# Performance work log

Hardware: AMD Instinct MI355X
Metric: run time of the kernel (lower is better)

Reference implementation:

```python
import jax, jax.numpy as jnp
import numpy as np

B, N_PER, D = 128, 512, 128        # graphs, nodes per graph, feature width
N = B * N_PER                      # 65536 total nodes
E = 524288                         # total edges (avg degree 8)
KS = (410, 328, 263)               # ceil(0.8*512), ceil(0.8*410), ceil(0.8*328)


def setup_inputs() -> dict:
    key = jax.random.key(0)
    ks = jax.random.split(key, 20)
    p = lambda k, shape: jax.random.normal(k, shape, jnp.float32) * 0.05
    rng = np.random.default_rng(0)
    g = rng.integers(0, B, size=E)
    s = rng.integers(0, N_PER, size=E)
    t = rng.integers(0, N_PER, size=E)
    edge_index = jnp.asarray(np.stack([g * N_PER + s, g * N_PER + t]).astype(np.int32))
    inp = {
        'x': jax.random.normal(ks[0], (N, 1, D), jnp.float32),
        'edge_index': edge_index,
    }
    i = 1
    for l in (1, 2, 3):
        inp[f'conv{l}_wl'] = p(ks[i], (D, D)); i += 1   # SAGEConv lin_l (neighbors) weight
        inp[f'conv{l}_bl'] = p(ks[i], (D,));  i += 1   # SAGEConv lin_l bias
        inp[f'conv{l}_wr'] = p(ks[i], (D, D)); i += 1   # SAGEConv lin_r (root) weight
        inp[f'pool{l}_w'] = p(ks[i], (D,));   i += 1   # TopKPooling score vector
    inp['lin1_w'] = p(ks[13], (128, 256)); inp['lin1_b'] = p(ks[14], (128,))
    inp['lin2_w'] = p(ks[15], (64, 128));  inp['lin2_b'] = p(ks[16], (64,))
    inp['lin3_w'] = p(ks[17], (1, 64));    inp['lin3_b'] = p(ks[18], (1,))
    return inp


def _sage(x, node_mask, src, dst, wl, bl, wr):
    # SAGEConv, mean aggregation: lin_l(mean_{j->i} x_j) + lin_r(x_i)
    em = (node_mask[src] & node_mask[dst]).astype(x.dtype)   # [E] valid-edge mask
    msum = jax.ops.segment_sum(x[src] * em[:, None], dst, num_segments=N)
    deg = jax.ops.segment_sum(em, dst, num_segments=N)
    mean = msum / jnp.maximum(deg, 1.0)[:, None]
    return mean @ wl.T + bl + x @ wr.T


def _topk_pool(x, node_mask, w, k):
    # TopKPooling: score = x.w/||w||; keep top-k per graph; gate kept x by tanh(score)
    score = (x @ w) / (jnp.linalg.norm(w) + 1e-16)           # [N]
    score = jnp.where(node_mask, score, -jnp.inf)
    _, idx = jax.lax.top_k(score.reshape(B, N_PER), k)       # [B, k] within-graph ids
    nm = jnp.zeros((B, N_PER), bool).at[jnp.arange(B)[:, None], idx].set(True).reshape(-1)
    x = jnp.where(nm[:, None], x * jnp.tanh(score)[:, None], 0.0)
    return x, nm


def _readout(x, node_mask, k):
    # cat([global_max_pool, global_mean_pool]) over the k surviving nodes per graph
    xb = x.reshape(B, N_PER, -1)
    mb = node_mask.reshape(B, N_PER, 1)
    gmax = jnp.max(jnp.where(mb, xb, -jnp.inf), axis=1)
    gmean = jnp.sum(jnp.where(mb, xb, 0.0), axis=1) / k
    return jnp.concatenate([gmax, gmean], axis=1)            # [B, 2D]


def _forward(edge_index, x, conv1_wl, conv1_bl, conv1_wr, pool1_w,
             conv2_wl, conv2_bl, conv2_wr, pool2_w,
             conv3_wl, conv3_bl, conv3_wr, pool3_w,
             lin1_w, lin1_b, lin2_w, lin2_b, lin3_w, lin3_b):
    src, dst = edge_index[0], edge_index[1]
    h = x[:, 0, :]                                           # x.squeeze(1) -> [N, D]
    nm = jnp.ones((N,), bool)
    layers = ((conv1_wl, conv1_bl, conv1_wr, pool1_w),
              (conv2_wl, conv2_bl, conv2_wr, pool2_w),
              (conv3_wl, conv3_bl, conv3_wr, pool3_w))
    reads = []
    for (wl, bl, wr, pw), k in zip(layers, KS):
        h = jax.nn.relu(_sage(h, nm, src, dst, wl, bl, wr))
        h, nm = _topk_pool(h, nm, pw, k)
        reads.append(_readout(h, nm, float(k)))
    z = reads[0] + reads[1] + reads[2]                       # [B, 256]
    z = jax.nn.relu(z @ lin1_w.T + lin1_b)
    z = jax.nn.relu(z @ lin2_w.T + lin2_b)
    # dropout p=0.5 is a no-op at eval time
    return jax.nn.sigmoid(z @ lin3_w.T + lin3_b)[:, 0]       # [B]


def reference(x, edge_index, conv1_wl, conv1_bl, conv1_wr, pool1_w,
              conv2_wl, conv2_bl, conv2_wr, pool2_w,
              conv3_wl, conv3_bl, conv3_wr, pool3_w,
              lin1_w, lin1_b, lin2_w, lin2_b, lin3_w, lin3_b):
    return _forward(edge_index, x, conv1_wl, conv1_bl, conv1_wr, pool1_w,
                    conv2_wl, conv2_bl, conv2_wr, pool2_w,
                    conv3_wl, conv3_bl, conv3_wr, pool3_w,
                    lin1_w, lin1_b, lin2_w, lin2_b, lin3_w, lin3_b)
```

## Files before the change

kernel.cpp:

```cpp
#include <hip/hip_runtime.h>
#include <math.h>

#define NND 65536
#define NPER 512
#define NGR 128
#define DD 128
#define NED 524288

typedef __attribute__((ext_vector_type(8))) short short8;
typedef __attribute__((ext_vector_type(4))) float f32x4;

__device__ __forceinline__ unsigned short f2b(float f) {
  unsigned u = __float_as_uint(f);
  return (unsigned short)((u + 0x7FFFu + ((u >> 16) & 1u)) >> 16);
}
__device__ __forceinline__ float b2f(unsigned short h) {
  return __uint_as_float(((unsigned)h) << 16);
}


__global__ __launch_bounds__(256) void init_kernel(int* __restrict__ counts,
                                                   float2* __restrict__ tm) {
  int i = blockIdx.x * 256 + threadIdx.x;
  counts[i] = 0;
  tm[i] = make_float2(1.f, 1.f);
}

__global__ __launch_bounds__(256) void hist_kernel(const int* __restrict__ ei,
                                                   int* __restrict__ counts) {
  int e = blockIdx.x * 256 + threadIdx.x;
  atomicAdd(&counts[ei[NED + e]], 1);
}

__global__ __launch_bounds__(1024) void scan_kernel(const int* __restrict__ counts,
                                                    int* __restrict__ off,
                                                    int* __restrict__ cursor) {
  __shared__ int part[1024];
  int t = threadIdx.x;
  int base = t * 64;
  int s = 0;
  const int4* c4 = (const int4*)(counts + base);
  for (int i = 0; i < 16; ++i) {
    int4 v = c4[i];
    s += v.x + v.y + v.z + v.w;
  }
  part[t] = s;
  __syncthreads();
  for (int d = 1; d < 1024; d <<= 1) {
    int v = (t >= d) ? part[t - d] : 0;
    __syncthreads();
    part[t] += v;
    __syncthreads();
  }
  int run = (t == 0) ? 0 : part[t - 1];
  for (int i = 0; i < 64; ++i) {
    off[base + i] = run;
    cursor[base + i] = run;
    run += counts[base + i];
  }
  if (t == 1023) off[NND] = run;
}

__global__ __launch_bounds__(256) void scatter_kernel(const int* __restrict__ ei,
                                                      int* __restrict__ cursor,
                                                      int* __restrict__ ssrc) {
  int e = blockIdx.x * 256 + threadIdx.x;
  int dst = ei[NED + e];
  int pos = atomicAdd(&cursor[dst], 1);
  ssrc[pos] = ei[e];
}


__global__ __launch_bounds__(256) void prepw_kernel(
    const float* __restrict__ wl0, const float* __restrict__ wr0,
    const float* __restrict__ wl1, const float* __restrict__ wr1,
    const float* __restrict__ wl2, const float* __restrict__ wr2,
    unsigned short* __restrict__ Whi, unsigned short* __restrict__ Wlo) {
  const float* wls[3] = {wl0, wl1, wl2};
  const float* wrs[3] = {wr0, wr1, wr2};
  int e = blockIdx.x * 256 + threadIdx.x;
  int l = e >> 15;
  int o = e & 32767;
  int j = o & 7;
  int lane = (o >> 3) & 63;
  int nt = (o >> 9) & 7;
  int kc = o >> 12;
  int li = lane & 15, q = lane >> 4;
  int n = nt * 16 + li;
  int k = kc * 32 + q * 8 + j;
  const float* src = (k < 128) ? wls[l] : wrs[l];
  float v = src[n * DD + (k & 127)];
  unsigned short hi = f2b(v);
  float lo = v - b2f(hi);
  Whi[e] = hi;
  Wlo[e] = f2b(lo);
}


template <int CM>
__global__ __launch_bounds__(256) void agg_kernel_t(const float* __restrict__ x,
                                                    const float2* __restrict__ tm,
                                                    const int* __restrict__ off,
                                                    const int* __restrict__ ssrc,
                                                    float* __restrict__ mean) {
  const int wave = threadIdx.x >> 6;
  const int lane = threadIdx.x & 63;
  const int half = lane >> 5;
  const int l = lane & 31;
  const int bid = blockIdx.x;
  const int xcd = bid & 7;
  const int slot = bid >> 3;
  const int graph = xcd * 16 + (slot >> 7);
  const int within = slot & 127;
  const int dst = graph * NPER + within * 4 + wave;

  if (CM && tm[dst].x == 0.f) {
    if (lane < 32) *(float4*)(mean + (size_t)dst * DD + l * 4) = make_float4(0.f, 0.f, 0.f, 0.f);
    return;
  }
  const int beg = off[dst], end = off[dst + 1];
  float4 acc = make_float4(0.f, 0.f, 0.f, 0.f);
  int deg = 0;
  for (int base = beg; base < end; base += 64) {
    const int n = min(64, end - base);
    int sv = 0;
    float tv = 0.f;
    int live = 0;
    if (lane < n) {
      sv = ssrc[base + lane];
      if (CM) {
        const float2 mt = tm[sv];
        live = (mt.x != 0.f);
        tv = mt.y;
      }
    }
    if (CM)
      deg += (int)__popcll(__ballot(live));
    else
      deg += n;
    int j = half;
    for (; j + 6 < n; j += 8) {
      const int s0 = __shfl(sv, j);
      const int s1 = __shfl(sv, j + 2);
      const int s2 = __shfl(sv, j + 4);
      const int s3 = __shfl(sv, j + 6);
      const float4 v0 = *(const float4*)(x + (size_t)s0 * DD + l * 4);
      const float4 v1 = *(const float4*)(x + (size_t)s1 * DD + l * 4);
      const float4 v2 = *(const float4*)(x + (size_t)s2 * DD + l * 4);
      const float4 v3 = *(const float4*)(x + (size_t)s3 * DD + l * 4);
      if (CM) {
        const float t0 = __shfl(tv, j), t1 = __shfl(tv, j + 2);
        const float t2 = __shfl(tv, j + 4), t3 = __shfl(tv, j + 6);
        acc.x += v0.x * t0 + v1.x * t1 + v2.x * t2 + v3.x * t3;
        acc.y += v0.y * t0 + v1.y * t1 + v2.y * t2 + v3.y * t3;
        acc.z += v0.z * t0 + v1.z * t1 + v2.z * t2 + v3.z * t3;
        acc.w += v0.w * t0 + v1.w * t1 + v2.w * t2 + v3.w * t3;
      } else {
        acc.x += v0.x + v1.x + v2.x + v3.x;
        acc.y += v0.y + v1.y + v2.y + v3.y;
        acc.z += v0.z + v1.z + v2.z + v3.z;
        acc.w += v0.w + v1.w + v2.w + v3.w;
      }
    }
    for (; j < n; j += 2) {
      const int s = __shfl(sv, j);
      const float4 v = *(const float4*)(x + (size_t)s * DD + l * 4);
      if (CM) {
        const float t = __shfl(tv, j);
        acc.x += v.x * t;
        acc.y += v.y * t;
        acc.z += v.z * t;
        acc.w += v.w * t;
      } else {
        acc.x += v.x;
        acc.y += v.y;
        acc.z += v.z;
        acc.w += v.w;
      }
    }
  }
  acc.x += __shfl(acc.x, lane ^ 32);
  acc.y += __shfl(acc.y, lane ^ 32);
  acc.z += __shfl(acc.z, lane ^ 32);
  acc.w += __shfl(acc.w, lane ^ 32);
  const float inv = 1.f / (float)max(deg, 1);
  if (lane < 32) {
    float4 m;
    m.x = acc.x * inv;
    m.y = acc.y * inv;
    m.z = acc.z * inv;
    m.w = acc.w * inv;
    *(float4*)(mean + (size_t)dst * DD + l * 4) = m;
  }
}


#define GBM 64

template <int SCALE>
__global__ __launch_bounds__(256) void gemm_kernel_t(
    const float* __restrict__ Amean, const float* __restrict__ Ax,
    const float2* __restrict__ tmp,
    const unsigned short* __restrict__ Whi, const unsigned short* __restrict__ Wlo,
    const float* __restrict__ bias, const float* __restrict__ pw,
    float* __restrict__ outp, float* __restrict__ sraw) {
  __shared__ short Ah[2048];
  __shared__ short Al[2048];
  __shared__ float s_sp[4][GBM];
  const int tid = threadIdx.x;
  const int wv = tid >> 6;
  const int lane = tid & 63;
  const int q = lane >> 4;
  const int li = lane & 15;
  const int row0 = blockIdx.x * GBM;

  int sdst[2];
#pragma unroll
  for (int i = 0; i < 2; ++i) {
    const int id = tid + i * 256;
    const int r = id >> 3;
    const int kb = (id & 7) << 2;
    sdst[i] = ((r >> 4) * 64 + (kb >> 3) * 16 + (r & 15)) * 8 + (kb & 7);
  }

  f32x4 acc[4][2];
#pragma unroll
  for (int m = 0; m < 4; ++m)
#pragma unroll
    for (int n = 0; n < 2; ++n) acc[m][n] = (f32x4){0.f, 0.f, 0.f, 0.f};

  float4 pa[2];
  short8 pbh[2], pbl[2];

#define LOADA(KC)                                                                    \
  {                                                                                  \
    const float* Asrc = ((KC) < 4) ? Amean : Ax;                                     \
    const int cb = ((KC) & 3) * 32;                                                  \
    _Pragma("unroll") for (int i = 0; i < 2; ++i) {                                  \
      const int id = tid + i * 256;                                                  \
      pa[i] = *(const float4*)(Asrc + (size_t)(row0 + (id >> 3)) * DD + cb + ((id & 7) << 2)); \
      if (SCALE && (KC) >= 4) {                                                      \
        const float tt = tmp[row0 + (id >> 3)].y;                                    \
        pa[i].x *= tt; pa[i].y *= tt; pa[i].z *= tt; pa[i].w *= tt;                   \
      }                                                                              \
    }                                                                                \
  }
#define LOADB(KC)                                                                    \
  {                                                                                  \
    _Pragma("unroll") for (int n = 0; n < 2; ++n) {                                  \
      const int ga = (((KC)*8 + wv * 2 + n) * 64 + lane) * 8;                        \
      pbh[n] = *(const short8*)(Whi + ga);                                           \
      pbl[n] = *(const short8*)(Wlo + ga);                                           \
    }                                                                                \
  }

  LOADA(0) LOADB(0)

#pragma unroll
  for (int kc = 0; kc < 8; ++kc) {
#pragma unroll
    for (int i = 0; i < 2; ++i) {
      ushort4 hv, lv;
      hv.x = f2b(pa[i].x); lv.x = f2b(pa[i].x - b2f(hv.x));
      hv.y = f2b(pa[i].y); lv.y = f2b(pa[i].y - b2f(hv.y));
      hv.z = f2b(pa[i].z); lv.z = f2b(pa[i].z - b2f(hv.z));
      hv.w = f2b(pa[i].w); lv.w = f2b(pa[i].w - b2f(hv.w));
      *(ushort4*)(Ah + sdst[i]) = hv;
      *(ushort4*)(Al + sdst[i]) = lv;
    }
    short8 bh[2], bl[2];
    bh[0] = pbh[0]; bh[1] = pbh[1];
    bl[0] = pbl[0]; bl[1] = pbl[1];
    __syncthreads();
    short8 ah[4], al[4];
#pragma unroll
    for (int m = 0; m < 4; ++m) {
      ah[m] = *(const short8*)(Ah + (m * 64 + lane) * 8);
      al[m] = *(const short8*)(Al + (m * 64 + lane) * 8);
    }
    if (kc < 7) { LOADA(kc + 1) LOADB(kc + 1) }
#pragma unroll
    for (int m = 0; m < 4; ++m)
#pragma unroll
      for (int n = 0; n < 2; ++n) {
        acc[m][n] = __builtin_amdgcn_mfma_f32_16x16x32_bf16(ah[m], bh[n], acc[m][n], 0, 0, 0);
        acc[m][n] = __builtin_amdgcn_mfma_f32_16x16x32_bf16(ah[m], bl[n], acc[m][n], 0, 0, 0);
        acc[m][n] = __builtin_amdgcn_mfma_f32_16x16x32_bf16(al[m], bh[n], acc[m][n], 0, 0, 0);
      }
    __syncthreads();
  }
#undef LOADA
#undef LOADB

  const int c0 = wv * 32 + li;
  const int c1 = wv * 32 + 16 + li;
  const float b0 = bias[c0], b1 = bias[c1];
  const float p0 = pw[c0], p1 = pw[c1];
  float sp[16];
#pragma unroll
  for (int m = 0; m < 4; ++m) {
#pragma unroll
    for (int i = 0; i < 4; ++i) {
      const int r = row0 + m * 16 + q * 4 + i;
      const float v0 = fmaxf(acc[m][0][i] + b0, 0.f);
      const float v1 = fmaxf(acc[m][1][i] + b1, 0.f);
      outp[(size_t)r * DD + c0] = v0;
      outp[(size_t)r * DD + c1] = v1;
      sp[m * 4 + i] = v0 * p0 + v1 * p1;
    }
  }
#pragma unroll
  for (int e = 0; e < 16; ++e) {
    sp[e] += __shfl_xor(sp[e], 1);
    sp[e] += __shfl_xor(sp[e], 2);
    sp[e] += __shfl_xor(sp[e], 4);
    sp[e] += __shfl_xor(sp[e], 8);
  }
  if (li == 0) {
#pragma unroll
    for (int e = 0; e < 16; ++e) s_sp[wv][(e >> 2) * 16 + q * 4 + (e & 3)] = sp[e];
  }
  __syncthreads();
  if (tid < GBM)
    sraw[row0 + tid] = s_sp[0][tid] + s_sp[1][tid] + s_sp[2][tid] + s_sp[3][tid];
}


__global__ __launch_bounds__(256) void pool_kernel(const float* __restrict__ h,
                                                   const float* __restrict__ sraw,
                                                   const float* __restrict__ pw,
                                                   const float2* __restrict__ tmP,
                                                   float2* __restrict__ tmN,
                                                   float* __restrict__ zp,
                                                   const int kk) {
  __shared__ float s_sc[NPER];
  __shared__ float s_t[128];
  __shared__ unsigned char s_sel[128];
  __shared__ int s_rk[256];
  __shared__ float4 red4[512];
  __shared__ float s_norm;
  const int b = blockIdx.x;
  const int g = b >> 2;
  const int q = b & 3;
  const int tid = threadIdx.x;
  const int lane = tid & 63;

  if (tid < 64) {
    const float v0 = pw[lane], v1 = pw[lane + 64];
    float p = v0 * v0 + v1 * v1;
#pragma unroll
    for (int o = 32; o > 0; o >>= 1) p += __shfl_down(p, o);
    if (lane == 0) s_norm = 1.f / (sqrtf(p) + 1e-16f);
  }
  __syncthreads();
  const float inv_norm = s_norm;
#pragma unroll
  for (int i = 0; i < 2; ++i) {
    const int n = tid + i * 256;
    const int node = g * NPER + n;
    s_sc[n] = (tmP[node].x != 0.f) ? sraw[node] * inv_norm : -INFINITY;
  }
  __syncthreads();

  {
    const int n = q * 128 + (tid & 127);
    const int jb = (tid >> 7) * 256;
    const float s = s_sc[n];
    int rank = 0;
    for (int j = jb; j < jb + 256; ++j) {
      const float sj = s_sc[j];
      rank += (sj > s || (sj == s && j < n)) ? 1 : 0;
    }
    s_rk[tid] = rank;
  }
  __syncthreads();
  if (tid < 128) {
    const int n = q * 128 + tid;
    const int rank = s_rk[tid] + s_rk[tid + 128];
    const int sel = (rank < kk) ? 1 : 0;
    const float s = s_sc[n];
    const float t = sel ? tanhf(s) : 0.f;
    tmN[g * NPER + n] = make_float2(sel ? 1.f : 0.f, t);
    s_sel[tid] = (unsigned char)sel;
    s_t[tid] = t;
  }
  __syncthreads();

  const int c = tid & 31;
  const int r = tid >> 5;
  float4 pmax = make_float4(-INFINITY, -INFINITY, -INFINITY, -INFINITY);
  float4 psum = make_float4(0.f, 0.f, 0.f, 0.f);
  const size_t nbase = (size_t)g * NPER + q * 128;
  const float4* h4 = (const float4*)h;
  for (int i = 0; i < 16; ++i) {
    const int nl = r + 8 * i;
    if (s_sel[nl]) {
      float4 v = h4[(nbase + nl) * 32 + c];
      const float t = s_t[nl];
      v.x *= t; v.y *= t; v.z *= t; v.w *= t;
      pmax.x = fmaxf(pmax.x, v.x);
      pmax.y = fmaxf(pmax.y, v.y);
      pmax.z = fmaxf(pmax.z, v.z);
      pmax.w = fmaxf(pmax.w, v.w);
      psum.x += v.x; psum.y += v.y; psum.z += v.z; psum.w += v.w;
    }
  }
  red4[r * 32 + c] = pmax;
  red4[256 + r * 32 + c] = psum;
  __syncthreads();
  if (tid < 32) {
    float4 m = red4[tid];
    float4 sm = red4[256 + tid];
#pragma unroll
    for (int rr = 1; rr < 8; ++rr) {
      const float4 a = red4[rr * 32 + tid];
      const float4 s2 = red4[256 + rr * 32 + tid];
      m.x = fmaxf(m.x, a.x); m.y = fmaxf(m.y, a.y);
      m.z = fmaxf(m.z, a.z); m.w = fmaxf(m.w, a.w);
      sm.x += s2.x; sm.y += s2.y; sm.z += s2.z; sm.w += s2.w;
    }
    *(float4*)(zp + (size_t)b * 256 + tid * 4) = m;
    *(float4*)(zp + (size_t)b * 256 + 128 + tid * 4) = sm;
  }
}


__global__ __launch_bounds__(128) void mlp_kernel(const float* __restrict__ zpart,
                                                  const float* __restrict__ w1,
                                                  const float* __restrict__ b1,
                                                  const float* __restrict__ w2,
                                                  const float* __restrict__ b2,
                                                  const float* __restrict__ w3,
                                                  const float* __restrict__ b3,
                                                  float* __restrict__ out,
                                                  const float ik0, const float ik1,
                                                  const float ik2) {
  __shared__ float z[256];
  __shared__ float h1[128];
  __shared__ float h2[64];
  const int g = blockIdx.x;
  const int t = threadIdx.x;
  const float iks[3] = {ik0, ik1, ik2};
  float zmax = 0.f, zmean = 0.f;
#pragma unroll
  for (int l = 0; l < 3; ++l) {
    const float* zp = zpart + ((size_t)l * 512 + g * 4) * 256;
    zmax += fmaxf(fmaxf(zp[t], zp[256 + t]), fmaxf(zp[512 + t], zp[768 + t]));
    zmean += (zp[128 + t] + zp[384 + t] + zp[640 + t] + zp[896 + t]) * iks[l];
  }
  z[t] = zmax;
  z[128 + t] = zmean;
  __syncthreads();
  float a = b1[t];
  for (int k = 0; k < 256; ++k) a = fmaf(z[k], w1[t * 256 + k], a);
  h1[t] = fmaxf(a, 0.f);
  __syncthreads();
  if (t < 64) {
    float a2 = b2[t];
    for (int k = 0; k < 128; ++k) a2 = fmaf(h1[k], w2[t * 128 + k], a2);
    h2[t] = fmaxf(a2, 0.f);
  }
  __syncthreads();
  if (t == 0) {
    float a3 = b3[0];
    for (int k = 0; k < 64; ++k) a3 = fmaf(h2[k], w3[k], a3);
    out[g] = 1.f / (1.f + expf(-a3));
  }
}


extern "C" void kernel_launch(void* const* d_in, const int* in_sizes, int n_in,
                              void* d_out, int out_size, void* d_ws, size_t ws_size,
                              hipStream_t stream) {
  (void)in_sizes; (void)n_in; (void)out_size; (void)ws_size;
  const float* x_in = (const float*)d_in[0];
  const int* ei = (const int*)d_in[1];
  const float* wl[3] = {(const float*)d_in[2], (const float*)d_in[6], (const float*)d_in[10]};
  const float* cbl[3] = {(const float*)d_in[3], (const float*)d_in[7], (const float*)d_in[11]};
  const float* wr[3] = {(const float*)d_in[4], (const float*)d_in[8], (const float*)d_in[12]};
  const float* pw[3] = {(const float*)d_in[5], (const float*)d_in[9], (const float*)d_in[13]};
  const float* l1w = (const float*)d_in[14];
  const float* l1b = (const float*)d_in[15];
  const float* l2w = (const float*)d_in[16];
  const float* l2b = (const float*)d_in[17];
  const float* l3w = (const float*)d_in[18];
  const float* l3b = (const float*)d_in[19];
  float* out = (float*)d_out;

  char* w = (char*)d_ws;
  int* counts = (int*)(w + 0 * (1 << 20));
  int* off = (int*)(w + 1 * (1 << 20));
  int* cursor = (int*)(w + 2 * (1 << 20));
  float* sraw = (float*)(w + 2 * (1 << 20));
  float2* tmA = (float2*)(w + 3 * (1 << 20));
  float2* tmB = (float2*)(w + 3 * (1 << 20) + (1 << 19));
  float* zpart = (float*)(w + 4 * (1 << 20));
  unsigned short* Whi = (unsigned short*)(w + 5 * (1 << 20) + (1 << 19));
  unsigned short* Wlo = (unsigned short*)(w + 5 * (1 << 20) + 3 * (1 << 18));
  int* ssrc = (int*)(w + 6 * (1 << 20));
  float* mean = (float*)(w + (size_t)8 * (1 << 20));
  float* hA = (float*)(w + (size_t)40 * (1 << 20));
  float* hB = (float*)(w + (size_t)72 * (1 << 20));

  init_kernel<<<NND / 256, 256, 0, stream>>>(counts, tmA);
  hist_kernel<<<NED / 256, 256, 0, stream>>>(ei, counts);
  scan_kernel<<<1, 1024, 0, stream>>>(counts, off, cursor);
  scatter_kernel<<<NED / 256, 256, 0, stream>>>(ei, cursor, ssrc);
  prepw_kernel<<<384, 256, 0, stream>>>(wl[0], wr[0], wl[1], wr[1], wl[2], wr[2], Whi, Wlo);

  const int ks[3] = {410, 328, 263};
  const float* xl = x_in;
  float* houts[3] = {hA, hB, hA};
  float2* tprev[3] = {tmA, tmB, tmA};
  float2* tnext[3] = {tmB, tmA, tmB};
  for (int l = 0; l < 3; ++l) {
    float* hout = houts[l];
    if (l == 0) {
      agg_kernel_t<0><<<NND / 4, 256, 0, stream>>>(xl, tprev[l], off, ssrc, mean);
      gemm_kernel_t<0><<<NND / GBM, 256, 0, stream>>>(mean, xl, tprev[l],
                                                      Whi + (size_t)l * 32768,
                                                      Wlo + (size_t)l * 32768, cbl[l], pw[l],
                                                      hout, sraw);
    } else {
      agg_kernel_t<1><<<NND / 4, 256, 0, stream>>>(xl, tprev[l], off, ssrc, mean);
      gemm_kernel_t<1><<<NND / GBM, 256, 0, stream>>>(mean, xl, tprev[l],
                                                      Whi + (size_t)l * 32768,
                                                      Wlo + (size_t)l * 32768, cbl[l], pw[l],
                                                      hout, sraw);
    }
    pool_kernel<<<NGR * 4, 256, 0, stream>>>(hout, sraw, pw[l], tprev[l], tnext[l],
                                             zpart + (size_t)l * 512 * 256, ks[l]);
    xl = hout;
  }
  mlp_kernel<<<NGR, 128, 0, stream>>>(zpart, l1w, l1b, l2w, l2b, l3w, l3b, out,
                                      1.f / 410.f, 1.f / 328.f, 1.f / 263.f);
}
```

Before: 420.0 us.

## Aggregate four destination nodes per wave and emit split-bf16 mean directly

The aggregation kernel now assigns four consecutive destination nodes to each wave. It loads their CSR edge ranges once and walks a shared 64-edge window, assigning edges to per-node accumulators through bitmask ranges. It writes the mean as hi/lo bf16 pairs, so the GEMM kernel loads them straight into shared memory and no longer converts that half of its A operand. This amortises per-node launch and index overhead and moves the fp32-to-bf16 split into the aggregation. In exchange it adds per-node loop control and possible lane underuse when degrees vary.

```diff
diff --git a/kernel.cpp b/kernel.cpp
--- a/kernel.cpp
+++ b/kernel.cpp
@@ -102,7 +102,8 @@
                                                     const float2* __restrict__ tm,
                                                     const int* __restrict__ off,
                                                     const int* __restrict__ ssrc,
-                                                    float* __restrict__ mean) {
+                                                    unsigned short* __restrict__ mhi,
+                                                    unsigned short* __restrict__ mlo) {
   const int wave = threadIdx.x >> 6;
   const int lane = threadIdx.x & 63;
   const int half = lane >> 5;
@@ -110,23 +111,43 @@
   const int bid = blockIdx.x;
   const int xcd = bid & 7;
   const int slot = bid >> 3;
-  const int graph = xcd * 16 + (slot >> 7);
-  const int within = slot & 127;
-  const int dst = graph * NPER + within * 4 + wave;
-
-  if (CM && tm[dst].x == 0.f) {
-    if (lane < 32) *(float4*)(mean + (size_t)dst * DD + l * 4) = make_float4(0.f, 0.f, 0.f, 0.f);
-    return;
-  }
-  const int beg = off[dst], end = off[dst + 1];
-  float4 acc = make_float4(0.f, 0.f, 0.f, 0.f);
-  int deg = 0;
-  for (int base = beg; base < end; base += 64) {
-    const int n = min(64, end - base);
+  const int graph = xcd * 16 + (slot >> 5);
+  const int within = slot & 31;
+  const int d0 = graph * NPER + within * 16 + wave * 4;
+
+  int offv = 0;
+  if (lane < 5) offv = off[d0 + lane];
+  float deadv = 1.f;
+  if (CM && lane < 4) deadv = tm[d0 + lane].x;
+  const int b0 = __shfl(offv, 0);
+  const int b1 = __shfl(offv, 1);
+  const int b2 = __shfl(offv, 2);
+  const int b3 = __shfl(offv, 3);
+  const int e3 = __shfl(offv, 4);
+  float dd[4];
+  if (CM) {
+    dd[0] = __shfl(deadv, 0);
+    dd[1] = __shfl(deadv, 1);
+    dd[2] = __shfl(deadv, 2);
+    dd[3] = __shfl(deadv, 3);
+  }
+  const int begs[4] = {b0, b1, b2, b3};
+  const int ends[4] = {b1, b2, b3, e3};
+
+  float4 acc[4];
+  int deg[4];
+#pragma unroll
+  for (int d = 0; d < 4; ++d) {
+    acc[d] = make_float4(0.f, 0.f, 0.f, 0.f);
+    deg[d] = 0;
+  }
+
+  for (int base = b0; base < e3; base += 64) {
+    const int nwin = min(64, e3 - base);
     int sv = 0;
     float tv = 0.f;
     int live = 0;
-    if (lane < n) {
+    if (lane < nwin) {
       sv = ssrc[base + lane];
       if (CM) {
         const float2 mt = tm[sv];
@@ -134,63 +155,89 @@
         tv = mt.y;
       }
     }
+    unsigned long long bl;
     if (CM)
-      deg += (int)__popcll(__ballot(live));
+      bl = __ballot(live);
     else
-      deg += n;
-    int j = half;
-    for (; j + 6 < n; j += 8) {
-      const int s0 = __shfl(sv, j);
-      const int s1 = __shfl(sv, j + 2);
-      const int s2 = __shfl(sv, j + 4);
-      const int s3 = __shfl(sv, j + 6);
-      const float4 v0 = *(const float4*)(x + (size_t)s0 * DD + l * 4);
-      const float4 v1 = *(const float4*)(x + (size_t)s1 * DD + l * 4);
-      const float4 v2 = *(const float4*)(x + (size_t)s2 * DD + l * 4);
-      const float4 v3 = *(const float4*)(x + (size_t)s3 * DD + l * 4);
-      if (CM) {
-        const float t0 = __shfl(tv, j), t1 = __shfl(tv, j + 2);
-        const float t2 = __shfl(tv, j + 4), t3 = __shfl(tv, j + 6);
-        acc.x += v0.x * t0 + v1.x * t1 + v2.x * t2 + v3.x * t3;
-        acc.y += v0.y * t0 + v1.y * t1 + v2.y * t2 + v3.y * t3;
-        acc.z += v0.z * t0 + v1.z * t1 + v2.z * t2 + v3.z * t3;
-        acc.w += v0.w * t0 + v1.w * t1 + v2.w * t2 + v3.w * t3;
-      } else {
-        acc.x += v0.x + v1.x + v2.x + v3.x;
-        acc.y += v0.y + v1.y + v2.y + v3.y;
-        acc.z += v0.z + v1.z + v2.z + v3.z;
-        acc.w += v0.w + v1.w + v2.w + v3.w;
+      bl = (nwin == 64) ? ~0ull : ((1ull << nwin) - 1);
+
+#pragma unroll
+    for (int d = 0; d < 4; ++d) {
+      if (CM && dd[d] == 0.f) continue;
+      const int lo = max(begs[d], base);
+      const int hi = min(ends[d], base + 64);
+      if (lo >= hi) continue;
+      const int j0 = lo - base;
+      const int j1 = hi - base;
+      const unsigned long long wm =
+          (((j1 == 64) ? ~0ull : ((1ull << j1) - 1)) & ~((1ull << j0) - 1));
+      deg[d] += (int)__popcll(bl & wm);
+      int j = j0 + half;
+      for (; j + 6 < j1; j += 8) {
+        const int s0 = __shfl(sv, j);
+        const int s1 = __shfl(sv, j + 2);
+        const int s2 = __shfl(sv, j + 4);
+        const int s3 = __shfl(sv, j + 6);
+        const float4 v0 = *(const float4*)(x + (size_t)s0 * DD + l * 4);
+        const float4 v1 = *(const float4*)(x + (size_t)s1 * DD + l * 4);
+        const float4 v2 = *(const float4*)(x + (size_t)s2 * DD + l * 4);
+        const float4 v3 = *(const float4*)(x + (size_t)s3 * DD + l * 4);
+        if (CM) {
+          const float t0 = __shfl(tv, j), t1 = __shfl(tv, j + 2);
+          const float t2 = __shfl(tv, j + 4), t3 = __shfl(tv, j + 6);
+          acc[d].x += v0.x * t0 + v1.x * t1 + v2.x * t2 + v3.x * t3;
+          acc[d].y += v0.y * t0 + v1.y * t1 + v2.y * t2 + v3.y * t3;
+          acc[d].z += v0.z * t0 + v1.z * t1 + v2.z * t2 + v3.z * t3;
+          acc[d].w += v0.w * t0 + v1.w * t1 + v2.w * t2 + v3.w * t3;
+        } else {
+          acc[d].x += v0.x + v1.x + v2.x + v3.x;
+          acc[d].y += v0.y + v1.y + v2.y + v3.y;
+          acc[d].z += v0.z + v1.z + v2.z + v3.z;
+          acc[d].w += v0.w + v1.w + v2.w + v3.w;
+        }
       }
-    }
-    for (; j < n; j += 2) {
-      const int s = __shfl(sv, j);
-      const float4 v = *(const float4*)(x + (size_t)s * DD + l * 4);
-      if (CM) {
-        const float t = __shfl(tv, j);
-        acc.x += v.x * t;
-        acc.y += v.y * t;
-        acc.z += v.z * t;
-        acc.w += v.w * t;
-      } else {
-        acc.x += v.x;
-        acc.y += v.y;
-        acc.z += v.z;
-        acc.w += v.w;
+      for (; j < j1; j += 2) {
+        const int s = __shfl(sv, j);
+        const float4 v = *(const float4*)(x + (size_t)s * DD + l * 4);
+        if (CM) {
+          const float t = __shfl(tv, j);
+          acc[d].x += v.x * t;
+          acc[d].y += v.y * t;
+          acc[d].z += v.z * t;
+          acc[d].w += v.w * t;
+        } else {
+          acc[d].x += v.x;
+          acc[d].y += v.y;
+          acc[d].z += v.z;
+          acc[d].w += v.w;
+        }
       }
     }
   }
-  acc.x += __shfl(acc.x, lane ^ 32);
-  acc.y += __shfl(acc.y, lane ^ 32);
-  acc.z += __shfl(acc.z, lane ^ 32);
-  acc.w += __shfl(acc.w, lane ^ 32);
-  const float inv = 1.f / (float)max(deg, 1);
-  if (lane < 32) {
-    float4 m;
-    m.x = acc.x * inv;
-    m.y = acc.y * inv;
-    m.z = acc.z * inv;
-    m.w = acc.w * inv;
-    *(float4*)(mean + (size_t)dst * DD + l * 4) = m;
+
+#pragma unroll
+  for (int d = 0; d < 4; ++d) {
+    float4 a = acc[d];
+    a.x += __shfl(a.x, lane ^ 32);
+    a.y += __shfl(a.y, lane ^ 32);
+    a.z += __shfl(a.z, lane ^ 32);
+    a.w += __shfl(a.w, lane ^ 32);
+    if (lane < 32) {
+      const float inv = 1.f / (float)max(deg[d], 1);
+      float4 m;
+      m.x = a.x * inv;
+      m.y = a.y * inv;
+      m.z = a.z * inv;
+      m.w = a.w * inv;
+      ushort4 hv, lv;
+      hv.x = f2b(m.x); lv.x = f2b(m.x - b2f(hv.x));
+      hv.y = f2b(m.y); lv.y = f2b(m.y - b2f(hv.y));
+      hv.z = f2b(m.z); lv.z = f2b(m.z - b2f(hv.z));
+      hv.w = f2b(m.w); lv.w = f2b(m.w - b2f(hv.w));
+      const size_t ad = (size_t)(d0 + d) * DD + l * 4;
+      *(ushort4*)(mhi + ad) = hv;
+      *(ushort4*)(mlo + ad) = lv;
+    }
   }
 }
 
@@ -199,8 +246,8 @@
 
 template <int SCALE>
 __global__ __launch_bounds__(256) void gemm_kernel_t(
-    const float* __restrict__ Amean, const float* __restrict__ Ax,
-    const float2* __restrict__ tmp,
+    const unsigned short* __restrict__ Amh, const unsigned short* __restrict__ Aml,
+    const float* __restrict__ Ax, const float2* __restrict__ tmp,
     const unsigned short* __restrict__ Whi, const unsigned short* __restrict__ Wlo,
     const float* __restrict__ bias, const float* __restrict__ pw,
     float* __restrict__ outp, float* __restrict__ sraw) {
@@ -230,43 +277,61 @@
     for (int n = 0; n < 2; ++n) acc[m][n] = (f32x4){0.f, 0.f, 0.f, 0.f};
 
   float4 pa[2];
+  ushort4 pmh[2], pml[2];
   short8 pbh[2], pbl[2];
 
-#define LOADA(KC)                                                                    \
-  {                                                                                  \
-    const float* Asrc = ((KC) < 4) ? Amean : Ax;                                     \
-    const int cb = ((KC) & 3) * 32;                                                  \
-    _Pragma("unroll") for (int i = 0; i < 2; ++i) {                                  \
-      const int id = tid + i * 256;                                                  \
-      pa[i] = *(const float4*)(Asrc + (size_t)(row0 + (id >> 3)) * DD + cb + ((id & 7) << 2)); \
-      if (SCALE && (KC) >= 4) {                                                      \
-        const float tt = tmp[row0 + (id >> 3)].y;                                    \
-        pa[i].x *= tt; pa[i].y *= tt; pa[i].z *= tt; pa[i].w *= tt;                   \
-      }                                                                              \
-    }                                                                                \
-  }
-#define LOADB(KC)                                                                    \
-  {                                                                                  \
-    _Pragma("unroll") for (int n = 0; n < 2; ++n) {                                  \
-      const int ga = (((KC)*8 + wv * 2 + n) * 64 + lane) * 8;                        \
-      pbh[n] = *(const short8*)(Whi + ga);                                           \
-      pbl[n] = *(const short8*)(Wlo + ga);                                           \
-    }                                                                                \
+#define LOADA(KC)                                                                      \
+  {                                                                                    \
+    if ((KC) < 4) {                                                                    \
+      const int cb = (KC)*32;                                                          \
+      _Pragma("unroll") for (int i = 0; i < 2; ++i) {                                  \
+        const int id = tid + i * 256;                                                  \
+        const size_t ga = (size_t)(row0 + (id >> 3)) * DD + cb + ((id & 7) << 2);      \
+        pmh[i] = *(const ushort4*)(Amh + ga);                                          \
+        pml[i] = *(const ushort4*)(Aml + ga);                                          \
+      }                                                                                \
+    } else {                                                                           \
+      const int cb = ((KC)&3) * 32;                                                    \
+      _Pragma("unroll") for (int i = 0; i < 2; ++i) {                                  \
+        const int id = tid + i * 256;                                                  \
+        pa[i] = *(const float4*)(Ax + (size_t)(row0 + (id >> 3)) * DD + cb + ((id & 7) << 2)); \
+        if (SCALE) {                                                                   \
+          const float tt = tmp[row0 + (id >> 3)].y;                                    \
+          pa[i].x *= tt; pa[i].y *= tt; pa[i].z *= tt; pa[i].w *= tt;                  \
+        }                                                                              \
+      }                                                                                \
+    }                                                                                  \
+  }
+#define LOADB(KC)                                                                      \
+  {                                                                                    \
+    _Pragma("unroll") for (int n = 0; n < 2; ++n) {                                    \
+      const int ga = (((KC)*8 + wv * 2 + n) * 64 + lane) * 8;                          \
+      pbh[n] = *(const short8*)(Whi + ga);                                             \
+      pbl[n] = *(const short8*)(Wlo + ga);                                             \
+    }                                                                                  \
   }
 
   LOADA(0) LOADB(0)
 
 #pragma unroll
   for (int kc = 0; kc < 8; ++kc) {
-#pragma unroll
-    for (int i = 0; i < 2; ++i) {
-      ushort4 hv, lv;
-      hv.x = f2b(pa[i].x); lv.x = f2b(pa[i].x - b2f(hv.x));
-      hv.y = f2b(pa[i].y); lv.y = f2b(pa[i].y - b2f(hv.y));
-      hv.z = f2b(pa[i].z); lv.z = f2b(pa[i].z - b2f(hv.z));
-      hv.w = f2b(pa[i].w); lv.w = f2b(pa[i].w - b2f(hv.w));
-      *(ushort4*)(Ah + sdst[i]) = hv;
-      *(ushort4*)(Al + sdst[i]) = lv;
+    if (kc < 4) {
+#pragma unroll
+      for (int i = 0; i < 2; ++i) {
+        *(ushort4*)(Ah + sdst[i]) = pmh[i];
+        *(ushort4*)(Al + sdst[i]) = pml[i];
+      }
+    } else {
+#pragma unroll
+      for (int i = 0; i < 2; ++i) {
+        ushort4 hv, lv;
+        hv.x = f2b(pa[i].x); lv.x = f2b(pa[i].x - b2f(hv.x));
+        hv.y = f2b(pa[i].y); lv.y = f2b(pa[i].y - b2f(hv.y));
+        hv.z = f2b(pa[i].z); lv.z = f2b(pa[i].z - b2f(hv.z));
+        hv.w = f2b(pa[i].w); lv.w = f2b(pa[i].w - b2f(hv.w));
+        *(ushort4*)(Ah + sdst[i]) = hv;
+        *(ushort4*)(Al + sdst[i]) = lv;
+      }
     }
     short8 bh[2], bl[2];
     bh[0] = pbh[0]; bh[1] = pbh[1];
@@ -278,7 +343,16 @@
       ah[m] = *(const short8*)(Ah + (m * 64 + lane) * 8);
       al[m] = *(const short8*)(Al + (m * 64 + lane) * 8);
     }
-    if (kc < 7) { LOADA(kc + 1) LOADB(kc + 1) }
+    switch (kc) {
+      case 0: LOADA(1) LOADB(1) break;
+      case 1: LOADA(2) LOADB(2) break;
+      case 2: LOADA(3) LOADB(3) break;
+      case 3: LOADA(4) LOADB(4) break;
+      case 4: LOADA(5) LOADB(5) break;
+      case 5: LOADA(6) LOADB(6) break;
+      case 6: LOADA(7) LOADB(7) break;
+      default: break;
+    }
 #pragma unroll
     for (int m = 0; m < 4; ++m)
 #pragma unroll
@@ -498,7 +572,8 @@
   unsigned short* Whi = (unsigned short*)(w + 5 * (1 << 20) + (1 << 19));
   unsigned short* Wlo = (unsigned short*)(w + 5 * (1 << 20) + 3 * (1 << 18));
   int* ssrc = (int*)(w + 6 * (1 << 20));
-  float* mean = (float*)(w + (size_t)8 * (1 << 20));
+  unsigned short* mhi = (unsigned short*)(w + (size_t)8 * (1 << 20));
+  unsigned short* mlo = (unsigned short*)(w + (size_t)24 * (1 << 20));
   float* hA = (float*)(w + (size_t)40 * (1 << 20));
   float* hB = (float*)(w + (size_t)72 * (1 << 20));
 
@@ -516,14 +591,14 @@
   for (int l = 0; l < 3; ++l) {
     float* hout = houts[l];
     if (l == 0) {
-      agg_kernel_t<0><<<NND / 4, 256, 0, stream>>>(xl, tprev[l], off, ssrc, mean);
-      gemm_kernel_t<0><<<NND / GBM, 256, 0, stream>>>(mean, xl, tprev[l],
+      agg_kernel_t<0><<<4096, 256, 0, stream>>>(xl, tprev[l], off, ssrc, mhi, mlo);
+      gemm_kernel_t<0><<<NND / GBM, 256, 0, stream>>>(mhi, mlo, xl, tprev[l],
                                                       Whi + (size_t)l * 32768,
                                                       Wlo + (size_t)l * 32768, cbl[l], pw[l],
                                                       hout, sraw);
     } else {
-      agg_kernel_t<1><<<NND / 4, 256, 0, stream>>>(xl, tprev[l], off, ssrc, mean);
-      gemm_kernel_t<1><<<NND / GBM, 256, 0, stream>>>(mean, xl, tprev[l],
+      agg_kernel_t<1><<<4096, 256, 0, stream>>>(xl, tprev[l], off, ssrc, mhi, mlo);
+      gemm_kernel_t<1><<<NND / GBM, 256, 0, stream>>>(mhi, mlo, xl, tprev[l],
                                                       Whi + (size_t)l * 32768,
                                                       Wlo + (size_t)l * 32768, cbl[l], pw[l],
                                                       hout, sraw);
```

New measurement: 406.1 us. 3.3% less time.
